# Optimization experiments

Hardware: AMD Instinct MI355X
Metric: run time of the kernel (lower is better)

## Reference

```python
import jax, jax.numpy as jnp
import numpy as np

WS = 8          # window side
HEADS = 8
DH = 32         # dim_head
DIM = 256
INNER = DH * HEADS  # 256
SCALE = DH ** -0.5


def _window(t):
    # b (h b0) (w b1) c -> b (h w) (b0 b1) c
    b, H, W, c = t.shape
    t = t.reshape(b, H // WS, WS, W // WS, WS, c).transpose(0, 1, 3, 2, 4, 5)
    return t.reshape(b, (H // WS) * (W // WS), WS * WS, c)


def _unwindow(t, H, W):
    # b (h w) (b0 b1) c -> b (h b0) (w b1) c
    b, n, mm, c = t.shape
    t = t.reshape(b, H // WS, W // WS, WS, WS, c).transpose(0, 1, 3, 2, 4, 5)
    return t.reshape(b, H, W, c)


def _split_heads(t, nh):
    # b n mm (h d) -> b n h mm d
    b, n, mm, c = t.shape
    return t.reshape(b, n, mm, nh, c // nh).transpose(0, 1, 3, 2, 4)


def _merge_heads(t):
    # b n h mm d -> b n mm (h d)
    b, n, h, mm, d = t.shape
    return t.transpose(0, 1, 3, 2, 4).reshape(b, n, mm, h * d)


def _attn(q, k, v, pos):
    sim = jnp.einsum('bnhid,bnhjd->bnhij', q * SCALE, k) + pos
    a = jax.nn.softmax(sim, axis=-1)
    return jnp.einsum('bnhij,bnhjd->bnhid', a, v)


def setup_inputs() -> dict:
    key = jax.random.key(0)
    ks = jax.random.split(key, 6)
    B, S = 4, 128
    seq_l1 = WS * WS              # 64
    seq_l2 = S * S // seq_l1      # 256
    x = jax.random.normal(ks[0], (B, S, S, DIM), jnp.float32)
    Wq = jax.random.normal(ks[1], (DIM, INNER), jnp.float32) * 0.02
    Wkv = jax.random.normal(ks[2], (DIM, 2 * INNER), jnp.float32) * 0.02
    Wo = jax.random.normal(ks[3], (INNER, DIM), jnp.float32) * 0.02
    bo = jnp.zeros((DIM,), jnp.float32)
    pos_emb1 = jax.random.normal(ks[4], (1, 1, HEADS // 2, seq_l1, seq_l1), jnp.float32)
    pos_emb2 = jax.random.normal(ks[5], (1, 1, HEADS // 2, seq_l2, seq_l2), jnp.float32)
    return {"x": x, "Wq": Wq, "Wkv": Wkv, "Wo": Wo, "bo": bo,
            "pos_emb1": pos_emb1, "pos_emb2": pos_emb2}


def reference(x, Wq, Wkv, Wo, bo, pos_emb1, pos_emb2):
    b, H, W, _ = x.shape
    nh = HEADS // 2
    q = x @ Wq                      # [b,H,W,INNER]
    kv = x @ Wkv
    k, v = jnp.split(kv, 2, axis=-1)
    ch = INNER // 2
    q1, q2 = q[..., :ch], q[..., ch:]
    k1, k2 = k[..., :ch], k[..., ch:]
    v1, v2 = v[..., :ch], v[..., ch:]

    # --- local branch: attention within each 8x8 window ---
    q1, k1, v1 = (_split_heads(_window(t), nh) for t in (q1, k1, v1))
    out1 = _merge_heads(_attn(q1, k1, v1, pos_emb1))   # [b, nW, 64, ch]

    # --- global branch: attention across windows at fixed in-window position ---
    q2, k2, v2 = (_split_heads(_window(t).transpose(0, 2, 1, 3), nh)
                  for t in (q2, k2, v2))
    out2 = _merge_heads(_attn(q2, k2, v2, pos_emb2))   # [b, 64, nW, ch]
    out2 = out2.transpose(0, 2, 1, 3)                  # [b, nW, 64, ch]

    out = jnp.concatenate([out1, out2], axis=-1) @ Wo + bo
    return _unwindow(out, H, W)
```

## Files before the change

### kernel.cpp

```cpp
#include <hip/hip_runtime.h>
#include <hip/hip_bf16.h>
#include <stdint.h>


typedef float f32x4 __attribute__((ext_vector_type(4)));
typedef __bf16 bf16_t;
typedef __bf16 bf16x8 __attribute__((ext_vector_type(8)));
typedef __bf16 bf16x4 __attribute__((ext_vector_type(4)));
typedef __bf16 bf16x2 __attribute__((ext_vector_type(2)));

#define SCALE_F 0.17677669529663687f

__device__ __forceinline__ int token_of_row(int gr) {
  int b = gr >> 14, n = (gr >> 6) & 255, m = gr & 63;
  int h = ((n >> 4) << 3) + (m >> 3);
  int w = ((n & 15) << 3) + (m & 7);
  return ((b << 7) + h) * 128 + w;
}

__global__ __launch_bounds__(256) void prep_k(
    const float* __restrict__ Wq, const float* __restrict__ Wkv,
    const float* __restrict__ Wo, bf16_t* __restrict__ WqkvT,
    bf16_t* __restrict__ WoT) {
  int tid = blockIdx.x * 256 + threadIdx.x;
  if (tid < 196608) {
    int k = tid / 768, c = tid % 768;
    float v = (c < 256) ? Wq[k * 256 + c] : Wkv[k * 512 + (c - 256)];
    WqkvT[c * 256 + k] = (bf16_t)v;
  } else if (tid < 262144) {
    int t = tid - 196608;
    int k = t >> 8, c = t & 255;
    WoT[c * 256 + k] = (bf16_t)Wo[k * 256 + c];
  }
}

__global__ __launch_bounds__(256) void gemm_qkv_k(
    const float* __restrict__ x, const bf16_t* __restrict__ Wt,
    bf16_t* __restrict__ QKV) {
  __shared__ bf16_t As[128 * 32];
  __shared__ bf16_t Bs[128 * 32];
  const int tid = threadIdx.x;
  const int row0 = blockIdx.x * 128;
  const int col0 = blockIdx.y * 128;
  const int lane = tid & 63, wv = tid >> 6;
  const int wm = (wv >> 1) * 64, wn = (wv & 1) * 64;
  const int tr = tid >> 2, kb = (tid & 3) * 8;

  const float* asrc0 = x + token_of_row(row0 + tr) * 256 + kb;
  const float* asrc1 = x + token_of_row(row0 + tr + 64) * 256 + kb;
  const bf16_t* bsrc0 = Wt + (col0 + tr) * 256 + kb;
  const bf16_t* bsrc1 = Wt + (col0 + tr + 64) * 256 + kb;

  f32x4 acc[4][4];
#pragma unroll
  for (int m = 0; m < 4; ++m)
#pragma unroll
    for (int n = 0; n < 4; ++n) acc[m][n] = 0.f;

  for (int ks = 0; ks < 256; ks += 32) {
    __syncthreads();
    {
      const float* s0 = asrc0 + ks;
      const float* s1 = asrc1 + ks;
      f32x4 a0 = *(const f32x4*)s0, a1 = *(const f32x4*)(s0 + 4);
      f32x4 b0 = *(const f32x4*)s1, b1 = *(const f32x4*)(s1 + 4);
      bf16x8 oa, ob;
      oa[0]=(bf16_t)a0[0]; oa[1]=(bf16_t)a0[1]; oa[2]=(bf16_t)a0[2]; oa[3]=(bf16_t)a0[3];
      oa[4]=(bf16_t)a1[0]; oa[5]=(bf16_t)a1[1]; oa[6]=(bf16_t)a1[2]; oa[7]=(bf16_t)a1[3];
      ob[0]=(bf16_t)b0[0]; ob[1]=(bf16_t)b0[1]; ob[2]=(bf16_t)b0[2]; ob[3]=(bf16_t)b0[3];
      ob[4]=(bf16_t)b1[0]; ob[5]=(bf16_t)b1[1]; ob[6]=(bf16_t)b1[2]; ob[7]=(bf16_t)b1[3];
      *(bf16x8*)&As[tr * 32 + kb] = oa;
      *(bf16x8*)&As[(tr + 64) * 32 + kb] = ob;
      *(int4*)&Bs[tr * 32 + kb] = *(const int4*)(bsrc0 + ks);
      *(int4*)&Bs[(tr + 64) * 32 + kb] = *(const int4*)(bsrc1 + ks);
    }
    __syncthreads();
    bf16x8 aF[4], bF[4];
#pragma unroll
    for (int m = 0; m < 4; ++m)
      aF[m] = *(const bf16x8*)&As[(wm + m * 16 + (lane & 15)) * 32 + (lane >> 4) * 8];
#pragma unroll
    for (int n = 0; n < 4; ++n)
      bF[n] = *(const bf16x8*)&Bs[(wn + n * 16 + (lane & 15)) * 32 + (lane >> 4) * 8];
#pragma unroll
    for (int m = 0; m < 4; ++m)
#pragma unroll
      for (int n = 0; n < 4; ++n)
        acc[m][n] = __builtin_amdgcn_mfma_f32_16x16x32_bf16(aF[m], bF[n], acc[m][n], 0, 0, 0);
  }

#pragma unroll
  for (int m = 0; m < 4; ++m) {
#pragma unroll
    for (int r = 0; r < 4; ++r) {
      int grow = row0 + wm + m * 16 + ((lane >> 4) << 2) + r;
      bf16_t* dst = QKV + (size_t)grow * 768 + col0 + wn + (lane & 15);
#pragma unroll
      for (int n = 0; n < 4; ++n) dst[n * 16] = (bf16_t)acc[m][n][r];
    }
  }
}

__global__ __launch_bounds__(256, 3) void attn1_k(
    const bf16_t* __restrict__ QKV, const float* __restrict__ pos1,
    bf16_t* __restrict__ O) {
  __shared__ char lds[47104];
  const int bid = blockIdx.x;
  const int n = bid & 255, b = bid >> 8;
  const int tid = threadIdx.x;
  const int lane = tid & 63, h = tid >> 6;
  const int g = lane >> 4, c = lane & 15;
  char* Pw = lds + 38912 + h * 2048;
  const size_t rowbase = (size_t)(b * 256 + n) * 64;
  const char* base = (const char*)QKV + rowbase * 1536;

#pragma unroll
  for (int it = 0; it < 4; ++it) {
    int idx = it * 256 + tid;
    int hh = idx >> 8, key = (idx >> 2) & 63, ch4 = idx & 3;
    int4 kk = *(const int4*)(base + (size_t)key * 1536 + 512 + 64 * hh + ch4 * 16);
    *(int4*)(lds + (hh * 64 + key) * 80 + ch4 * 16) = kk;
  }
#pragma unroll
  for (int it = 0; it < 4; ++it) {
    int idx = it * 256 + tid;
    int hh = idx >> 8, mm = (idx >> 2) & 63, dq = idx & 3;
    bf16x8 vv = *(const bf16x8*)(base + (size_t)mm * 1536 + 1024 + 64 * hh + dq * 16);
#pragma unroll
    for (int j = 0; j < 8; ++j)
      *(bf16_t*)(lds + 20480 + hh * 4608 + (dq * 8 + j) * 144 + mm * 2) = vv[j];
  }

  bf16x8 qa[4];
#pragma unroll
  for (int qf = 0; qf < 4; ++qf)
    qa[qf] = *(const bf16x8*)(base + (size_t)(qf * 16 + c) * 1536 + 64 * h + 16 * g);
  __syncthreads();

  bf16x8 kfr[4];
#pragma unroll
  for (int kf = 0; kf < 4; ++kf)
    kfr[kf] = *(const bf16x8*)(lds + (h * 64 + kf * 16 + c) * 80 + 16 * g);
  bf16x8 vfr[2][2];
#pragma unroll
  for (int kb = 0; kb < 2; ++kb)
#pragma unroll
    for (int dt = 0; dt < 2; ++dt)
      vfr[kb][dt] = *(const bf16x8*)(lds + 20480 + h * 4608 + (dt * 16 + c) * 144 + kb * 64 + g * 16);

  f32x4 Ov[2][4];
#pragma unroll
  for (int dt = 0; dt < 2; ++dt)
#pragma unroll
    for (int qf = 0; qf < 4; ++qf) Ov[dt][qf] = 0.f;

#pragma unroll
  for (int qf = 0; qf < 4; ++qf) {
    f32x4 S[4];
#pragma unroll
    for (int kf = 0; kf < 4; ++kf) {
      S[kf] = 0.f;
      S[kf] = __builtin_amdgcn_mfma_f32_16x16x32_bf16(kfr[kf], qa[qf], S[kf], 0, 0, 0);
    }
    const float* pp = pos1 + ((h * 64 + qf * 16 + c) * 64 + 4 * g);
#pragma unroll
    for (int kf = 0; kf < 4; ++kf) {
      f32x4 pv = *(const f32x4*)(pp + kf * 16);
      S[kf] = S[kf] * SCALE_F + pv;
    }
    float tm0 = fmaxf(fmaxf(S[0][0], S[0][1]), fmaxf(S[0][2], S[0][3]));
    float tm1 = fmaxf(fmaxf(S[1][0], S[1][1]), fmaxf(S[1][2], S[1][3]));
    float tm2 = fmaxf(fmaxf(S[2][0], S[2][1]), fmaxf(S[2][2], S[2][3]));
    float tm3 = fmaxf(fmaxf(S[3][0], S[3][1]), fmaxf(S[3][2], S[3][3]));
    float t = fmaxf(fmaxf(tm0, tm1), fmaxf(tm2, tm3));
    t = fmaxf(t, __shfl_xor(t, 16));
    t = fmaxf(t, __shfl_xor(t, 32));
    float ls = 0.f;
#pragma unroll
    for (int kf = 0; kf < 4; ++kf)
#pragma unroll
      for (int r = 0; r < 4; ++r) {
        S[kf][r] = __expf(S[kf][r] - t);
        ls += S[kf][r];
      }
    ls += __shfl_xor(ls, 16);
    ls += __shfl_xor(ls, 32);
    float inv = 1.0f / ls;
#pragma unroll
    for (int kf = 0; kf < 4; ++kf)
#pragma unroll
      for (int p = 0; p < 2; ++p) {
        bf16x2 w;
        w[0] = (bf16_t)(S[kf][2 * p] * inv);
        w[1] = (bf16_t)(S[kf][2 * p + 1] * inv);
        int byteo = c * 128 + kf * 32 + g * 8 + p * 4;
        *(bf16x2*)(Pw + (byteo ^ ((c & 7) << 4))) = w;
      }
    bf16x8 pb0 = *(const bf16x8*)(Pw + ((c * 128 + g * 16) ^ ((c & 7) << 4)));
    bf16x8 pb1 = *(const bf16x8*)(Pw + ((c * 128 + 64 + g * 16) ^ ((c & 7) << 4)));
    Ov[0][qf] = __builtin_amdgcn_mfma_f32_16x16x32_bf16(vfr[0][0], pb0, Ov[0][qf], 0, 0, 0);
    Ov[1][qf] = __builtin_amdgcn_mfma_f32_16x16x32_bf16(vfr[0][1], pb0, Ov[1][qf], 0, 0, 0);
    Ov[0][qf] = __builtin_amdgcn_mfma_f32_16x16x32_bf16(vfr[1][0], pb1, Ov[0][qf], 0, 0, 0);
    Ov[1][qf] = __builtin_amdgcn_mfma_f32_16x16x32_bf16(vfr[1][1], pb1, Ov[1][qf], 0, 0, 0);
  }

#pragma unroll
  for (int qf = 0; qf < 4; ++qf)
#pragma unroll
    for (int dt = 0; dt < 2; ++dt) {
      int row = (b * 256 + n) * 64 + qf * 16 + c;
      bf16x4 ov;
      ov[0] = (bf16_t)Ov[dt][qf][0]; ov[1] = (bf16_t)Ov[dt][qf][1];
      ov[2] = (bf16_t)Ov[dt][qf][2]; ov[3] = (bf16_t)Ov[dt][qf][3];
      *(bf16x4*)(O + (size_t)row * 256 + 32 * h + dt * 16 + 4 * g) = ov;
    }
}

__global__ __launch_bounds__(256, 3) void attn2_k(
    const bf16_t* __restrict__ QKV, const float* __restrict__ pos2,
    bf16_t* __restrict__ O) {
  __shared__ char lds[45568];
  const int bid = blockIdx.x;
  const int h = bid & 3, m = (bid >> 2) & 63, b = bid >> 8;
  const int tid = threadIdx.x;
  const int lane = tid & 63, wid = tid >> 6;
  const int g = lane >> 4, c = lane & 15;
  char* Pw = lds + 37376 + wid * 2048;
  const char* kvbase = (const char*)QKV + (size_t)(b * 16384 + m) * 1536;

#pragma unroll
  for (int it = 0; it < 4; ++it) {
    int idx = it * 256 + tid;
    int key = idx >> 2, ch4 = idx & 3;
    int4 kk = *(const int4*)(kvbase + (size_t)key * 98304 + 768 + 64 * h + ch4 * 16);
    *(int4*)(lds + key * 80 + ch4 * 16) = kk;
  }
#pragma unroll
  for (int it = 0; it < 4; ++it) {
    int idx = it * 256 + tid;
    int nn = idx >> 2, dq = idx & 3;
    bf16x8 vv = *(const bf16x8*)(kvbase + (size_t)nn * 98304 + 1280 + 64 * h + dq * 16);
#pragma unroll
    for (int j = 0; j < 8; ++j)
      *(bf16_t*)(lds + 20480 + (dq * 8 + j) * 528 + nn * 2) = vv[j];
  }

  bf16x8 qa[4];
#pragma unroll
  for (int qf = 0; qf < 4; ++qf)
    qa[qf] = *(const bf16x8*)((const char*)QKV +
        (size_t)((b * 256 + wid * 64 + qf * 16 + c) * 64 + m) * 1536 + 256 + 64 * h + 16 * g);
  __syncthreads();

  f32x4 Ov[2][4];
  float mrun[4], lrun[4];
#pragma unroll
  for (int qf = 0; qf < 4; ++qf) {
    Ov[0][qf] = 0.f; Ov[1][qf] = 0.f;
    mrun[qf] = -3.0e38f; lrun[qf] = 0.f;
  }

  for (int kt = 0; kt < 4; ++kt) {
    bf16x8 kfr[4];
#pragma unroll
    for (int kf = 0; kf < 4; ++kf)
      kfr[kf] = *(const bf16x8*)(lds + (kt * 64 + kf * 16 + c) * 80 + 16 * g);
    bf16x8 vfr[2][2];
#pragma unroll
    for (int kb = 0; kb < 2; ++kb)
#pragma unroll
      for (int dt = 0; dt < 2; ++dt)
        vfr[kb][dt] = *(const bf16x8*)(lds + 20480 + (dt * 16 + c) * 528 + kt * 128 + kb * 64 + g * 16);

#pragma unroll
    for (int qf = 0; qf < 4; ++qf) {
      f32x4 S[4];
#pragma unroll
      for (int kf = 0; kf < 4; ++kf) {
        S[kf] = 0.f;
        S[kf] = __builtin_amdgcn_mfma_f32_16x16x32_bf16(kfr[kf], qa[qf], S[kf], 0, 0, 0);
      }
      const float* pp = pos2 + ((h * 256 + wid * 64 + qf * 16 + c) * 256 + kt * 64 + 4 * g);
#pragma unroll
      for (int kf = 0; kf < 4; ++kf) {
        f32x4 pv = *(const f32x4*)(pp + kf * 16);
        S[kf] = S[kf] * SCALE_F + pv;
      }
      float tm0 = fmaxf(fmaxf(S[0][0], S[0][1]), fmaxf(S[0][2], S[0][3]));
      float tm1 = fmaxf(fmaxf(S[1][0], S[1][1]), fmaxf(S[1][2], S[1][3]));
      float tm2 = fmaxf(fmaxf(S[2][0], S[2][1]), fmaxf(S[2][2], S[2][3]));
      float tm3 = fmaxf(fmaxf(S[3][0], S[3][1]), fmaxf(S[3][2], S[3][3]));
      float t = fmaxf(fmaxf(tm0, tm1), fmaxf(tm2, tm3));
      t = fmaxf(t, __shfl_xor(t, 16));
      t = fmaxf(t, __shfl_xor(t, 32));
      float mo = mrun[qf];
      float mn = fmaxf(mo, t);
      float rsc = __expf(mo - mn);
      mrun[qf] = mn;
      float ls = 0.f;
#pragma unroll
      for (int kf = 0; kf < 4; ++kf)
#pragma unroll
        for (int r = 0; r < 4; ++r) {
          S[kf][r] = __expf(S[kf][r] - mn);
          ls += S[kf][r];
        }
      ls += __shfl_xor(ls, 16);
      ls += __shfl_xor(ls, 32);
      lrun[qf] = lrun[qf] * rsc + ls;
      Ov[0][qf] *= rsc;
      Ov[1][qf] *= rsc;
#pragma unroll
      for (int kf = 0; kf < 4; ++kf)
#pragma unroll
        for (int p = 0; p < 2; ++p) {
          bf16x2 w;
          w[0] = (bf16_t)S[kf][2 * p];
          w[1] = (bf16_t)S[kf][2 * p + 1];
          int byteo = c * 128 + kf * 32 + g * 8 + p * 4;
          *(bf16x2*)(Pw + (byteo ^ ((c & 7) << 4))) = w;
        }
      bf16x8 pb0 = *(const bf16x8*)(Pw + ((c * 128 + g * 16) ^ ((c & 7) << 4)));
      bf16x8 pb1 = *(const bf16x8*)(Pw + ((c * 128 + 64 + g * 16) ^ ((c & 7) << 4)));
      Ov[0][qf] = __builtin_amdgcn_mfma_f32_16x16x32_bf16(vfr[0][0], pb0, Ov[0][qf], 0, 0, 0);
      Ov[1][qf] = __builtin_amdgcn_mfma_f32_16x16x32_bf16(vfr[0][1], pb0, Ov[1][qf], 0, 0, 0);
      Ov[0][qf] = __builtin_amdgcn_mfma_f32_16x16x32_bf16(vfr[1][0], pb1, Ov[0][qf], 0, 0, 0);
      Ov[1][qf] = __builtin_amdgcn_mfma_f32_16x16x32_bf16(vfr[1][1], pb1, Ov[1][qf], 0, 0, 0);
    }
  }

#pragma unroll
  for (int qf = 0; qf < 4; ++qf) {
    float inv = 1.0f / lrun[qf];
    int qrow = (b * 256 + wid * 64 + qf * 16 + c) * 64 + m;
#pragma unroll
    for (int dt = 0; dt < 2; ++dt) {
      bf16x4 ov;
      ov[0] = (bf16_t)(Ov[dt][qf][0] * inv); ov[1] = (bf16_t)(Ov[dt][qf][1] * inv);
      ov[2] = (bf16_t)(Ov[dt][qf][2] * inv); ov[3] = (bf16_t)(Ov[dt][qf][3] * inv);
      *(bf16x4*)(O + (size_t)qrow * 256 + 128 + 32 * h + dt * 16 + 4 * g) = ov;
    }
  }
}

__global__ __launch_bounds__(256) void gemm_out_k(
    const bf16_t* __restrict__ A, const bf16_t* __restrict__ Wt,
    const float* __restrict__ bo, float* __restrict__ out) {
  __shared__ bf16_t As[128 * 32];
  __shared__ bf16_t Bs[128 * 32];
  const int tid = threadIdx.x;
  const int row0 = blockIdx.x * 128;
  const int col0 = blockIdx.y * 128;
  const int lane = tid & 63, wv = tid >> 6;
  const int wm = (wv >> 1) * 64, wn = (wv & 1) * 64;
  const int tr = tid >> 2, kb = (tid & 3) * 8;

  const bf16_t* asrc0 = A + (size_t)(row0 + tr) * 256 + kb;
  const bf16_t* asrc1 = A + (size_t)(row0 + tr + 64) * 256 + kb;
  const bf16_t* bsrc0 = Wt + (col0 + tr) * 256 + kb;
  const bf16_t* bsrc1 = Wt + (col0 + tr + 64) * 256 + kb;

  f32x4 acc[4][4];
#pragma unroll
  for (int m = 0; m < 4; ++m)
#pragma unroll
    for (int n = 0; n < 4; ++n) acc[m][n] = 0.f;

  for (int ks = 0; ks < 256; ks += 32) {
    __syncthreads();
    *(int4*)&As[tr * 32 + kb] = *(const int4*)(asrc0 + ks);
    *(int4*)&As[(tr + 64) * 32 + kb] = *(const int4*)(asrc1 + ks);
    *(int4*)&Bs[tr * 32 + kb] = *(const int4*)(bsrc0 + ks);
    *(int4*)&Bs[(tr + 64) * 32 + kb] = *(const int4*)(bsrc1 + ks);
    __syncthreads();
    bf16x8 aF[4], bF[4];
#pragma unroll
    for (int m = 0; m < 4; ++m)
      aF[m] = *(const bf16x8*)&As[(wm + m * 16 + (lane & 15)) * 32 + (lane >> 4) * 8];
#pragma unroll
    for (int n = 0; n < 4; ++n)
      bF[n] = *(const bf16x8*)&Bs[(wn + n * 16 + (lane & 15)) * 32 + (lane >> 4) * 8];
#pragma unroll
    for (int m = 0; m < 4; ++m)
#pragma unroll
      for (int n = 0; n < 4; ++n)
        acc[m][n] = __builtin_amdgcn_mfma_f32_16x16x32_bf16(aF[m], bF[n], acc[m][n], 0, 0, 0);
  }

  float bias[4];
#pragma unroll
  for (int n = 0; n < 4; ++n) bias[n] = bo[col0 + wn + n * 16 + (lane & 15)];

#pragma unroll
  for (int m = 0; m < 4; ++m) {
#pragma unroll
    for (int r = 0; r < 4; ++r) {
      int grow = row0 + wm + m * 16 + ((lane >> 4) << 2) + r;
      int tok = token_of_row(grow);
      float* dst = out + (size_t)tok * 256 + col0 + wn + (lane & 15);
#pragma unroll
      for (int n = 0; n < 4; ++n) dst[n * 16] = acc[m][n][r] + bias[n];
    }
  }
}

extern "C" void kernel_launch(void* const* d_in, const int* in_sizes, int n_in,
                              void* d_out, int out_size, void* d_ws, size_t ws_size,
                              hipStream_t stream) {
  (void)in_sizes; (void)n_in; (void)out_size; (void)ws_size;
  const float* x    = (const float*)d_in[0];
  const float* Wq   = (const float*)d_in[1];
  const float* Wkv  = (const float*)d_in[2];
  const float* Wo   = (const float*)d_in[3];
  const float* bo   = (const float*)d_in[4];
  const float* pos1 = (const float*)d_in[5];
  const float* pos2 = (const float*)d_in[6];
  float* out = (float*)d_out;

  char* ws = (char*)d_ws;
  bf16_t* WqkvT = (bf16_t*)(ws);
  bf16_t* WoT   = (bf16_t*)(ws + 393216);
  bf16_t* QKVb  = (bf16_t*)(ws + 524288);
  bf16_t* attnO = (bf16_t*)(ws + 101187584ull);

  prep_k<<<1024, 256, 0, stream>>>(Wq, Wkv, Wo, WqkvT, WoT);
  dim3 g1(512, 6);
  gemm_qkv_k<<<g1, 256, 0, stream>>>(x, WqkvT, QKVb);
  attn1_k<<<1024, 256, 0, stream>>>(QKVb, pos1, attnO);
  attn2_k<<<1024, 256, 0, stream>>>(QKVb, pos2, attnO);
  dim3 g3(512, 2);
  gemm_out_k<<<g3, 256, 0, stream>>>(attnO, WoT, bo, out);
}
```

Measured before the change: 297.1 us.

## Stage full A tile once in LDS and loop over all QKV column chunks

The QKV GEMM now loads a block's 128 token rows of x (all 256 K) into swizzled LDS once, converting to bf16 a single time, and iterates over the six 128-wide output column chunks inside the block. This removes the sixfold re-reading and re-conversion of fp32 x across the old 6-wide grid. The B tiles are also swizzled to reduce LDS bank conflicts. In exchange the block uses about 80 KB of LDS and the grid shrinks to 512 blocks, which lowers occupancy and parallelism.

New measurement: 286.6 us. 1.04x faster.

```diff
diff --git a/kernel.cpp b/kernel.cpp
--- a/kernel.cpp
+++ b/kernel.cpp
@@ -34,69 +34,84 @@
   }
 }
 
-__global__ __launch_bounds__(256) void gemm_qkv_k(
+__global__ __launch_bounds__(256, 2) void gemm_qkv_k(
     const float* __restrict__ x, const bf16_t* __restrict__ Wt,
     bf16_t* __restrict__ QKV) {
-  __shared__ bf16_t As[128 * 32];
-  __shared__ bf16_t Bs[128 * 32];
+  __shared__ char lds[81920];
+  char* Bs = lds + 65536;
   const int tid = threadIdx.x;
   const int row0 = blockIdx.x * 128;
-  const int col0 = blockIdx.y * 128;
   const int lane = tid & 63, wv = tid >> 6;
   const int wm = (wv >> 1) * 64, wn = (wv & 1) * 64;
-  const int tr = tid >> 2, kb = (tid & 3) * 8;
-
-  const float* asrc0 = x + token_of_row(row0 + tr) * 256 + kb;
-  const float* asrc1 = x + token_of_row(row0 + tr + 64) * 256 + kb;
-  const bf16_t* bsrc0 = Wt + (col0 + tr) * 256 + kb;
-  const bf16_t* bsrc1 = Wt + (col0 + tr + 64) * 256 + kb;
-
-  f32x4 acc[4][4];
-#pragma unroll
-  for (int m = 0; m < 4; ++m)
-#pragma unroll
-    for (int n = 0; n < 4; ++n) acc[m][n] = 0.f;
-
-  for (int ks = 0; ks < 256; ks += 32) {
-    __syncthreads();
-    {
-      const float* s0 = asrc0 + ks;
-      const float* s1 = asrc1 + ks;
-      f32x4 a0 = *(const f32x4*)s0, a1 = *(const f32x4*)(s0 + 4);
-      f32x4 b0 = *(const f32x4*)s1, b1 = *(const f32x4*)(s1 + 4);
-      bf16x8 oa, ob;
-      oa[0]=(bf16_t)a0[0]; oa[1]=(bf16_t)a0[1]; oa[2]=(bf16_t)a0[2]; oa[3]=(bf16_t)a0[3];
-      oa[4]=(bf16_t)a1[0]; oa[5]=(bf16_t)a1[1]; oa[6]=(bf16_t)a1[2]; oa[7]=(bf16_t)a1[3];
-      ob[0]=(bf16_t)b0[0]; ob[1]=(bf16_t)b0[1]; ob[2]=(bf16_t)b0[2]; ob[3]=(bf16_t)b0[3];
-      ob[4]=(bf16_t)b1[0]; ob[5]=(bf16_t)b1[1]; ob[6]=(bf16_t)b1[2]; ob[7]=(bf16_t)b1[3];
-      *(bf16x8*)&As[tr * 32 + kb] = oa;
-      *(bf16x8*)&As[(tr + 64) * 32 + kb] = ob;
-      *(int4*)&Bs[tr * 32 + kb] = *(const int4*)(bsrc0 + ks);
-      *(int4*)&Bs[(tr + 64) * 32 + kb] = *(const int4*)(bsrc1 + ks);
-    }
-    __syncthreads();
-    bf16x8 aF[4], bF[4];
+  const int g = lane >> 4, c = lane & 15;
+
+#pragma unroll
+  for (int it = 0; it < 16; ++it) {
+    int u = it * 256 + tid;
+    int row = u >> 5;
+    int kf4 = (u & 31) * 8;
+    const float* src = x + (size_t)token_of_row(row0 + row) * 256 + kf4;
+    f32x4 a0 = *(const f32x4*)src;
+    f32x4 a1 = *(const f32x4*)(src + 4);
+    bf16x8 o;
+    o[0]=(bf16_t)a0[0]; o[1]=(bf16_t)a0[1]; o[2]=(bf16_t)a0[2]; o[3]=(bf16_t)a0[3];
+    o[4]=(bf16_t)a1[0]; o[5]=(bf16_t)a1[1]; o[6]=(bf16_t)a1[2]; o[7]=(bf16_t)a1[3];
+    int bo = (u & 31) * 16;
+    *(bf16x8*)(lds + row * 512 + (bo ^ ((row & 7) << 4))) = o;
+  }
+  __syncthreads();
+
+  for (int nc = 0; nc < 6; ++nc) {
+    f32x4 acc[4][4];
 #pragma unroll
     for (int m = 0; m < 4; ++m)
-      aF[m] = *(const bf16x8*)&As[(wm + m * 16 + (lane & 15)) * 32 + (lane >> 4) * 8];
-#pragma unroll
-    for (int n = 0; n < 4; ++n)
-      bF[n] = *(const bf16x8*)&Bs[(wn + n * 16 + (lane & 15)) * 32 + (lane >> 4) * 8];
-#pragma unroll
-    for (int m = 0; m < 4; ++m)
-#pragma unroll
-      for (int n = 0; n < 4; ++n)
-        acc[m][n] = __builtin_amdgcn_mfma_f32_16x16x32_bf16(aF[m], bF[n], acc[m][n], 0, 0, 0);
-  }
-
-#pragma unroll
-  for (int m = 0; m < 4; ++m) {
-#pragma unroll
-    for (int r = 0; r < 4; ++r) {
-      int grow = row0 + wm + m * 16 + ((lane >> 4) << 2) + r;
-      bf16_t* dst = QKV + (size_t)grow * 768 + col0 + wn + (lane & 15);
-#pragma unroll
-      for (int n = 0; n < 4; ++n) dst[n * 16] = (bf16_t)acc[m][n][r];
+#pragma unroll
+      for (int n = 0; n < 4; ++n) acc[m][n] = 0.f;
+
+    for (int kc = 0; kc < 4; ++kc) {
+#pragma unroll
+      for (int j = 0; j < 4; ++j) {
+        int unit = tid * 4 + j;
+        int col = unit >> 3, kp = unit & 7;
+        int4 w = *(const int4*)((const char*)Wt +
+            (size_t)(nc * 128 + col) * 512 + kc * 128 + kp * 16);
+        *(int4*)(Bs + col * 128 + ((kp * 16) ^ ((col & 7) << 4))) = w;
+      }
+      __syncthreads();
+
+#pragma unroll
+      for (int kf = 0; kf < 2; ++kf) {
+        bf16x8 aF[4], bF[4];
+        int kbyteA = kc * 128 + kf * 64 + g * 16;
+        int kbyteB = kf * 64 + g * 16;
+#pragma unroll
+        for (int m = 0; m < 4; ++m) {
+          int row = wm + m * 16 + c;
+          aF[m] = *(const bf16x8*)(lds + row * 512 + (kbyteA ^ ((row & 7) << 4)));
+        }
+#pragma unroll
+        for (int n = 0; n < 4; ++n) {
+          int col = wn + n * 16 + c;
+          bF[n] = *(const bf16x8*)(Bs + col * 128 + (kbyteB ^ ((col & 7) << 4)));
+        }
+#pragma unroll
+        for (int m = 0; m < 4; ++m)
+#pragma unroll
+          for (int n = 0; n < 4; ++n)
+            acc[m][n] = __builtin_amdgcn_mfma_f32_16x16x32_bf16(aF[m], bF[n], acc[m][n], 0, 0, 0);
+      }
+      __syncthreads();
+    }
+
+#pragma unroll
+    for (int m = 0; m < 4; ++m) {
+#pragma unroll
+      for (int r = 0; r < 4; ++r) {
+        int grow = row0 + wm + m * 16 + (g << 2) + r;
+        bf16_t* dst = QKV + (size_t)grow * 768 + nc * 128 + wn + c;
+#pragma unroll
+        for (int n = 0; n < 4; ++n) dst[n * 16] = (bf16_t)acc[m][n][r];
+      }
     }
   }
 }
@@ -424,8 +439,7 @@
   bf16_t* attnO = (bf16_t*)(ws + 101187584ull);
 
   prep_k<<<1024, 256, 0, stream>>>(Wq, Wkv, Wo, WqkvT, WoT);
-  dim3 g1(512, 6);
-  gemm_qkv_k<<<g1, 256, 0, stream>>>(x, WqkvT, QKVb);
+  gemm_qkv_k<<<512, 256, 0, stream>>>(x, WqkvT, QKVb);
   attn1_k<<<1024, 256, 0, stream>>>(QKVb, pos1, attnO);
   attn2_k<<<1024, 256, 0, stream>>>(QKVb, pos2, attnO);
   dim3 g3(512, 2);
```
